# Optimization experiments

Hardware: AMD Instinct MI355X
Metric: run time of the kernel (lower is better)

Reference implementation:

```python
import jax, jax.numpy as jnp
import numpy as np

N, E, ENC, EMB, PI = 100000, 1600000, 128, 128, 98
ALPHA1, ALPHA2 = 0.5, 0.5


def setup_inputs() -> dict:
    key = jax.random.key(0)
    ks = jax.random.split(key, 20)
    s = 0.05
    return {
        "x": jax.random.normal(ks[0], (N, ENC), jnp.float32),
        "d2an": jax.random.normal(ks[1], (N, PI), jnp.float32),
        "ei0": jax.random.randint(ks[2], (2, E), 0, N, jnp.int32),
        "ew0": jax.random.uniform(ks[3], (E,), jnp.float32, 0.1, 4.0),
        "ei1": jax.random.randint(ks[4], (2, E), 0, N, jnp.int32),
        "ew1": jax.random.uniform(ks[5], (E,), jnp.float32, 0.1, 4.0),
        "nodeW1": jax.random.normal(ks[6], (ENC, ENC + PI), jnp.float32) * s,
        "nodeW2": jax.random.normal(ks[7], (ENC, ENC + PI), jnp.float32) * s,
        "W1a": jax.random.normal(ks[8], (EMB, ENC), jnp.float32) * s,
        "W1b": jax.random.normal(ks[9], (EMB, ENC), jnp.float32) * s,
        "W2a": jax.random.normal(ks[10], (EMB, ENC), jnp.float32) * s,
        "W2b": jax.random.normal(ks[11], (EMB, ENC), jnp.float32) * s,
        "W3a": jax.random.normal(ks[12], (EMB, EMB), jnp.float32) * s,
        "W3b": jax.random.normal(ks[13], (EMB, EMB), jnp.float32) * s,
        "W4a": jax.random.normal(ks[14], (EMB, EMB), jnp.float32) * s,
        "W4b": jax.random.normal(ks[15], (EMB, EMB), jnp.float32) * s,
    }


def _layer(x, ei, ew, W1, W2, nodeW, d2an, first):
    """PosKnnGNNLayer.forward: add self loops, optional nodeLin, GCN deg norm +
    edge norm, gather -> lin1/lin2 -> scale -> scatter-add (aggr='add')."""
    n = x.shape[0]
    loop = jnp.arange(n, dtype=ei.dtype)
    row = jnp.concatenate([ei[0], loop])          # source nodes (x_j)
    col = jnp.concatenate([ei[1], loop])          # target nodes (aggregation)
    attr = jnp.concatenate([ew, jnp.ones((n,), ew.dtype)])  # self-loop fill=1.0
    if first:
        x = jnp.concatenate([x, d2an], axis=1) @ nodeW.T
    deg = jax.ops.segment_sum(jnp.ones_like(attr), col, num_segments=n)
    dis = jnp.where(deg > 0, jax.lax.rsqrt(jnp.maximum(deg, 1.0)), 0.0)
    deg_norm = dis[row] * dis[col]                # [E']
    einv = attr ** -0.5
    einv = jnp.where(jnp.isinf(einv), 0.0, einv)
    einv = jnp.minimum(einv, 1.0)                 # clamp >1 to 1
    h1 = x @ W1.T                                 # [N, out]
    h2 = x @ W2.T
    msg = deg_norm[:, None] * h1[row] + einv[:, None] * h2[row]  # [E', out]
    return jax.ops.segment_sum(msg, col, num_segments=n)


def reference(x, d2an, ei0, ew0, ei1, ew1, nodeW1, nodeW2,
              W1a, W1b, W2a, W2b, W3a, W3b, W4a, W4b):
    # eval mode: dropout(p=0.3) is identity
    x0 = jax.nn.relu(_layer(x, ei0, ew0, W1a, W1b, nodeW1, d2an, True))
    x1 = jax.nn.relu(_layer(x, ei1, ew1, W2a, W2b, nodeW2, d2an, True))
    xm = ALPHA1 * x0 + ALPHA2 * x1
    x0 = jax.nn.relu(_layer(xm, ei0, ew0, W3a, W3b, None, None, False))
    x1 = jax.nn.relu(_layer(xm, ei1, ew1, W4a, W4b, None, None, False))
    return ALPHA1 * x0 + ALPHA2 * x1
```

## Files before the change

kernel.cpp:

```cpp
#include <hip/hip_runtime.h>
#include <hip/hip_fp16.h>
#include <stdint.h>

#define NN 100000
#define NE 1600000
#define ETOT (NE + NN)
#define EPB 8192
#define NBLK ((NE + EPB - 1) / EPB)
#define NPB 512
#define NBUK ((NN + NPB - 1) / NPB)

typedef __attribute__((ext_vector_type(8))) short bf16x8;
typedef __attribute__((ext_vector_type(4))) float f32x4;
typedef __attribute__((ext_vector_type(4))) unsigned short us4;

__device__ __forceinline__ float bf2f(unsigned short u) {
    union { unsigned int i; float f; } x; x.i = ((unsigned int)u) << 16; return x.f;
}
__device__ __forceinline__ unsigned short f2bf(float f) {
    union { float f; unsigned int i; } x; x.f = f;
    unsigned int i = x.i;
    return (unsigned short)((i + 0x7FFFu + ((i >> 16) & 1u)) >> 16);
}
__device__ __forceinline__ int packab(float a, float b) {
    unsigned int ua = __half_as_ushort(__float2half_rn(a));
    unsigned int ub = __half_as_ushort(__float2half_rn(b));
    return (int)(ua | (ub << 16));
}
__device__ __forceinline__ float2 unpackab(int p) {
    float a = __half2float(__ushort_as_half((unsigned short)(p & 0xFFFF)));
    float b = __half2float(__ushort_as_half((unsigned short)(((unsigned int)p) >> 16)));
    return make_float2(a, b);
}

__global__ __launch_bounds__(256) void k_cnt(const int* ei0, const int* ei1, int* cntm) {
    __shared__ int h[NBUK];
    const int* col = (blockIdx.y ? ei1 : ei0) + NE;
    for (int i = threadIdx.x; i < NBUK; i += 256) h[i] = 0;
    __syncthreads();
    int base = blockIdx.x * EPB;
    for (int i = 0; i < EPB / 256; i++) {
        int e = base + i * 256 + threadIdx.x;
        if (e < NE) atomicAdd(&h[col[e] >> 9], 1);
    }
    __syncthreads();
    int* out = cntm + ((size_t)blockIdx.y * NBLK + blockIdx.x) * NBUK;
    for (int i = threadIdx.x; i < NBUK; i += 256) out[i] = h[i];
}

__global__ __launch_bounds__(256) void k_btot(const int* cntm, int* bstart, int* btot) {
    __shared__ int s[256];
    int t = threadIdx.x;
    const int* cnt = cntm + (size_t)blockIdx.y * NBLK * NBUK;
    int tot = 0;
    if (t < NBUK)
        for (int blk = 0; blk < NBLK; blk++) tot += cnt[(size_t)blk * NBUK + t];
    s[t] = tot; __syncthreads();
    for (int off = 1; off < 256; off <<= 1) {
        int u = (t >= off) ? s[t - off] : 0;
        __syncthreads(); s[t] += u; __syncthreads();
    }
    if (t < NBUK) {
        bstart[blockIdx.y * NBUK + t] = s[t] - tot;
        btot[blockIdx.y * NBUK + t] = tot;
    }
}

__global__ __launch_bounds__(256) void k_base2(const int* cntm, const int* bstart, int* basem) {
    __shared__ int s[256];
    int b = blockIdx.x;
    const int* cnt = cntm + (size_t)blockIdx.y * NBLK * NBUK;
    int t = threadIdx.x;
    int v = (t < NBLK) ? cnt[(size_t)t * NBUK + b] : 0;
    s[t] = v; __syncthreads();
    for (int off = 1; off < 256; off <<= 1) {
        int u = (t >= off) ? s[t - off] : 0;
        __syncthreads(); s[t] += u; __syncthreads();
    }
    if (t < NBLK)
        basem[((size_t)blockIdx.y * NBLK + t) * NBUK + b] =
            bstart[blockIdx.y * NBUK + b] + (s[t] - v);
}

__global__ __launch_bounds__(256) void k_scat1(const int* ei0, const float* ew0,
                                               const int* ei1, const float* ew1,
                                               const int* basem, int2* st0, int2* st1) {
    __shared__ int lb[NBUK];
    __shared__ int lc[NBUK];
    const int* er = blockIdx.y ? ei1 : ei0;
    const float* ew = blockIdx.y ? ew1 : ew0;
    int2* st = blockIdx.y ? st1 : st0;
    const int* bm = basem + ((size_t)blockIdx.y * NBLK + blockIdx.x) * NBUK;
    for (int i = threadIdx.x; i < NBUK; i += 256) { lb[i] = bm[i]; lc[i] = 0; }
    __syncthreads();
    int base = blockIdx.x * EPB;
    for (int i = 0; i < EPB / 256; i++) {
        int e = base + i * 256 + threadIdx.x;
        if (e >= NE) break;
        int r = er[e];
        int c = er[NE + e];
        float w = ew[e];
        int bkt = c >> 9;
        int rank = atomicAdd(&lc[bkt], 1);
        st[lb[bkt] + rank] = make_int2(r | ((c & 511) << 17), __float_as_int(w));
    }
}

__global__ __launch_bounds__(256) void k_deg(const int* bstart, const int* btot,
                                             const int2* st0, const int2* st1,
                                             int* deg0, int* deg1) {
    __shared__ int h[NPB];
    int b = blockIdx.x;
    const int2* st = blockIdx.y ? st1 : st0;
    int* deg = blockIdx.y ? deg1 : deg0;
    for (int i = threadIdx.x; i < NPB; i += 256) h[i] = 0;
    __syncthreads();
    int s0 = bstart[blockIdx.y * NBUK + b];
    int tot = btot[blockIdx.y * NBUK + b];
    for (int j = s0 + (int)threadIdx.x; j < s0 + tot; j += 256)
        atomicAdd(&h[(st[j].x >> 17) & 511], 1);
    __syncthreads();
    for (int i = threadIdx.x; i < NPB; i += 256) {
        int node = b * NPB + i;
        if (node < NN) deg[node] = h[i] + 1;
    }
}

__global__ void k_scan1(const int* deg0, const int* deg1, int* rp0, int* rp1s, int* bsum) {
    __shared__ int s[256];
    const int* deg = blockIdx.y ? deg1 : deg0;
    int* rp = (blockIdx.y ? rp1s : rp0) + 1;
    int* bs = bsum + blockIdx.y * 128;
    int tid = threadIdx.x;
    int base = blockIdx.x * 1024 + tid * 4;
    int v0 = 0, v1 = 0, v2 = 0, v3 = 0;
    if (base + 0 < NN) v0 = deg[base + 0];
    if (base + 1 < NN) v1 = deg[base + 1];
    if (base + 2 < NN) v2 = deg[base + 2];
    if (base + 3 < NN) v3 = deg[base + 3];
    int sum = v0 + v1 + v2 + v3;
    s[tid] = sum; __syncthreads();
    for (int off = 1; off < 256; off <<= 1) {
        int t = (tid >= off) ? s[tid - off] : 0;
        __syncthreads(); s[tid] += t; __syncthreads();
    }
    int run = s[tid] - sum;
    if (base + 0 < NN) { run += v0; rp[base + 0] = run; }
    if (base + 1 < NN) { run += v1; rp[base + 1] = run; }
    if (base + 2 < NN) { run += v2; rp[base + 2] = run; }
    if (base + 3 < NN) { run += v3; rp[base + 3] = run; }
    if (tid == 255) bs[blockIdx.x] = s[255];
}

__global__ void k_scan2(int* bsum, int nb) {
    __shared__ int s[128];
    int* bs = bsum + blockIdx.x * 128;
    int tid = threadIdx.x;
    int v = (tid < nb) ? bs[tid] : 0;
    s[tid] = v; __syncthreads();
    for (int off = 1; off < 128; off <<= 1) {
        int t = (tid >= off) ? s[tid - off] : 0;
        __syncthreads(); s[tid] += t; __syncthreads();
    }
    if (tid < nb) bs[tid] = s[tid] - v;
}

__global__ void k_scan3(int* rp0, int* rp1s, const int* bsum) {
    int* rowptr = blockIdx.y ? rp1s : rp0;
    int add = bsum[blockIdx.y * 128 + blockIdx.x];
    int tid = threadIdx.x;
    int base = blockIdx.x * 1024 + tid * 4;
    #pragma unroll
    for (int i = 0; i < 4; i++) {
        int idx = base + i;
        if (idx < NN) rowptr[idx + 1] += add;
    }
    if (blockIdx.x == 0 && tid == 0) rowptr[0] = 0;
}

__global__ void k_self(const int* rp0, const int* rp1s, const int* deg0, const int* deg1,
                       int2* eo0, int2* eo1, float* dis0, float* dis1) {
    int i = blockIdx.x * 256 + threadIdx.x;
    if (i >= NN) return;
    const int* rowptr = blockIdx.y ? rp1s : rp0;
    const int* deg = blockIdx.y ? deg1 : deg0;
    int2* eo = blockIdx.y ? eo1 : eo0;
    float* dis = blockIdx.y ? dis1 : dis0;
    int p = rowptr[i];
    float d = (float)deg[i];
    eo[p] = make_int2(i, packab(1.0f / d, 1.0f));
    dis[i] = rsqrtf(d);
}

__global__ __launch_bounds__(256) void k_scat2(const int* rp0, const int* rp1s,
                                               const int* bstart, const int* btot,
                                               const float* dis0, const float* dis1,
                                               const int2* st0, const int2* st1,
                                               int2* eo0, int2* eo1) {
    __shared__ int lcur[NPB];
    __shared__ float ldis[NPB];
    int b = blockIdx.x;
    const int* rowptr = blockIdx.y ? rp1s : rp0;
    const float* dis = blockIdx.y ? dis1 : dis0;
    const int2* st = blockIdx.y ? st1 : st0;
    int2* eo = blockIdx.y ? eo1 : eo0;
    int nstart = b * NPB;
    for (int i = threadIdx.x; i < NPB; i += 256) {
        int node = nstart + i;
        if (node < NN) { lcur[i] = rowptr[node] + 1; ldis[i] = dis[node]; }
    }
    __syncthreads();
    int s0 = bstart[blockIdx.y * NBUK + b];
    int tot = btot[blockIdx.y * NBUK + b];
    for (int j = s0 + (int)threadIdx.x; j < s0 + tot; j += 256) {
        int2 rec = st[j];
        int cl = (rec.x >> 17) & 511;
        int r  = rec.x & 0x1FFFF;
        float w = __int_as_float(rec.y);
        float a = dis[r] * ldis[cl];
        float bb = fminf(rsqrtf(w), 1.0f);
        int pos = atomicAdd(&lcur[cl], 1);
        eo[pos] = make_int2(r, packab(a, bb));
    }
}

__global__ void k_packx(const float* x, const float* d2, unsigned short* Xc) {
    int idx = blockIdx.x * 256 + threadIdx.x;
    if (idx >= NN * 64) return;
    int r = idx >> 6, k4 = (idx & 63) << 2;
    us4 o;
    if (k4 < 128) {
        float4 v = *(const float4*)(x + (size_t)r * 128 + k4);
        o[0] = f2bf(v.x); o[1] = f2bf(v.y); o[2] = f2bf(v.z); o[3] = f2bf(v.w);
    } else {
        #pragma unroll
        for (int i = 0; i < 4; i++) {
            int k = k4 + i;
            float v = (k < 226) ? d2[(size_t)r * 98 + (k - 128)] : 0.f;
            o[i] = f2bf(v);
        }
    }
    *(us4*)(Xc + (size_t)r * 256 + k4) = o;
}

__global__ void k_packw(const float* wn1, const float* wn2,
                        const float* w1a, const float* w1b,
                        const float* w2a, const float* w2b,
                        const float* w3a, const float* w3b,
                        const float* w4a, const float* w4b,
                        unsigned short* Wfnode, unsigned short* WfL) {
    int idx = blockIdx.x * 256 + threadIdx.x;
    if (idx < 65536) {
        int j = idx & 7, lane = (idx >> 3) & 63, ct = (idx >> 9) & 15, ks = idx >> 13;
        int k = ks * 32 + (lane >> 4) * 8 + j;
        int c = ct * 16 + (lane & 15);
        float v = 0.f;
        if (k < 226) v = (c < 128) ? wn1[c * 226 + k] : wn2[(c - 128) * 226 + k];
        Wfnode[idx] = f2bf(v);
    } else if (idx < 196608) {
        int li = idx - 65536;
        int set = li >> 15, r = li & 32767;
        const float* wa = (set == 0) ? w1a : (set == 1) ? w2a : (set == 2) ? w3a : w4a;
        const float* wb = (set == 0) ? w1b : (set == 1) ? w2b : (set == 2) ? w3b : w4b;
        int j = r & 7, lane = (r >> 3) & 63, ct = (r >> 9) & 7, ks = r >> 12;
        int k = ks * 32 + (lane >> 4) * 8 + j;
        int c = ct * 16 + (lane & 15);
        float v = (k < 128) ? wa[c * 128 + k] : wb[c * 128 + (k - 128)];
        WfL[li] = f2bf(v);
    }
}

template <int SRST, int SOFF>
__global__ __launch_bounds__(256) void k_agg(const unsigned short* S,
                                             const int* rowptr, const int2* eg,
                                             unsigned short* G) {
    int c = blockIdx.x * 4 + (threadIdx.x >> 6);
    int lane = threadIdx.x & 63;
    if (c >= NN) return;
    float a0 = 0.f, a1 = 0.f, b0 = 0.f, b1 = 0.f;
    int jb = rowptr[c], je = rowptr[c + 1];
    const unsigned short* Sb = S + SOFF + lane * 2;
    int j = jb;
    for (; j + 16 <= je; j += 16) {
        int2 e[16]; unsigned int u[16];
        #pragma unroll
        for (int i = 0; i < 16; i++) e[i] = eg[j + i];
        #pragma unroll
        for (int i = 0; i < 16; i++)
            u[i] = *(const unsigned int*)(Sb + (size_t)e[i].x * SRST);
        #pragma unroll
        for (int i = 0; i < 16; i++) {
            float2 w = unpackab(e[i].y);
            float x0 = bf2f((unsigned short)(u[i] & 0xFFFF));
            float x1 = bf2f((unsigned short)(u[i] >> 16));
            a0 += w.x * x0; a1 += w.x * x1; b0 += w.y * x0; b1 += w.y * x1;
        }
    }
    for (; j + 4 <= je; j += 4) {
        int2 e[4]; unsigned int u[4];
        #pragma unroll
        for (int i = 0; i < 4; i++) e[i] = eg[j + i];
        #pragma unroll
        for (int i = 0; i < 4; i++)
            u[i] = *(const unsigned int*)(Sb + (size_t)e[i].x * SRST);
        #pragma unroll
        for (int i = 0; i < 4; i++) {
            float2 w = unpackab(e[i].y);
            float x0 = bf2f((unsigned short)(u[i] & 0xFFFF));
            float x1 = bf2f((unsigned short)(u[i] >> 16));
            a0 += w.x * x0; a1 += w.x * x1; b0 += w.y * x0; b1 += w.y * x1;
        }
    }
    for (; j < je; j++) {
        int2 e = eg[j];
        unsigned int u = *(const unsigned int*)(Sb + (size_t)e.x * SRST);
        float2 w = unpackab(e.y);
        float x0 = bf2f((unsigned short)(u & 0xFFFF));
        float x1 = bf2f((unsigned short)(u >> 16));
        a0 += w.x * x0; a1 += w.x * x1; b0 += w.y * x0; b1 += w.y * x1;
    }
    unsigned int* gd = (unsigned int*)(G + (size_t)c * 256);
    gd[lane]      = (unsigned int)f2bf(a0) | ((unsigned int)f2bf(a1) << 16);
    gd[64 + lane] = (unsigned int)f2bf(b0) | ((unsigned int)f2bf(b1) << 16);
}

template <int MODE>
__global__ __launch_bounds__(256) void k_gemm(const unsigned short* A, int arst,
                                              const unsigned short* Wf, int nct_total,
                                              unsigned short* outB, float* outF,
                                              const unsigned short* T, int orst) {
    int wave = threadIdx.x >> 6, lane = threadIdx.x & 63;
    int m = lane & 15, quad = lane >> 4;
    int row0 = blockIdx.x * 64 + wave * 16;
    int arow = row0 + m;
    bool rowok = arow < NN;
    const unsigned short* Ap = A + (size_t)arow * arst + quad * 8;
    int ctbase = blockIdx.y * 8;
    f32x4 acc[8];
    #pragma unroll
    for (int t = 0; t < 8; t++) acc[t] = (f32x4){0.f, 0.f, 0.f, 0.f};

    #pragma unroll
    for (int ks = 0; ks < 8; ks++) {
        bf16x8 a;
        if (rowok) a = *(const bf16x8*)(Ap + ks * 32);
        else       a = (bf16x8){0, 0, 0, 0, 0, 0, 0, 0};
        const unsigned short* wp = Wf + ((size_t)(ks * nct_total + ctbase) * 64 + lane) * 8;
        #pragma unroll
        for (int t = 0; t < 8; t++) {
            bf16x8 b = *(const bf16x8*)(wp + t * 512);
            acc[t] = __builtin_amdgcn_mfma_f32_16x16x32_bf16(a, b, acc[t], 0, 0, 0);
        }
    }

    int col0 = blockIdx.y * 128;
    #pragma unroll
    for (int t = 0; t < 8; t++) {
        int c = col0 + t * 16 + m;
        #pragma unroll
        for (int rg = 0; rg < 4; rg++) {
            int r = row0 + quad * 4 + rg;
            if (r < NN) {
                float v = acc[t][rg];
                if (MODE == 0) {
                    outB[(size_t)r * orst + c] = f2bf(v);
                } else {
                    float tv = bf2f(T[(size_t)r * 128 + c]);
                    float o = 0.5f * fmaxf(tv, 0.f) + 0.5f * fmaxf(v, 0.f);
                    if (MODE == 1) outB[(size_t)r * orst + c] = f2bf(o);
                    else           outF[(size_t)r * 128 + c] = o;
                }
            }
        }
    }
}

extern "C" void kernel_launch(void* const* d_in, const int* in_sizes, int n_in,
                              void* d_out, int out_size, void* d_ws, size_t ws_size,
                              hipStream_t stream) {
    const float* x      = (const float*)d_in[0];
    const float* d2an   = (const float*)d_in[1];
    const int*   ei0    = (const int*)d_in[2];
    const float* ew0    = (const float*)d_in[3];
    const int*   ei1    = (const int*)d_in[4];
    const float* ew1    = (const float*)d_in[5];
    const float* nodeW1 = (const float*)d_in[6];
    const float* nodeW2 = (const float*)d_in[7];
    const float* W1a = (const float*)d_in[8],  *W1b = (const float*)d_in[9];
    const float* W2a = (const float*)d_in[10], *W2b = (const float*)d_in[11];
    const float* W3a = (const float*)d_in[12], *W3b = (const float*)d_in[13];
    const float* W4a = (const float*)d_in[14], *W4b = (const float*)d_in[15];
    float* out = (float*)d_out;

    char* p = (char*)d_ws;
    auto alloc = [&](size_t bytes) -> char* {
        char* r = p; p += (bytes + 255) & ~(size_t)255; return r;
    };
    unsigned short* bufA   = (unsigned short*)alloc((size_t)NN * 256 * 2);
    unsigned short* bufB   = (unsigned short*)alloc((size_t)NN * 256 * 2);
    unsigned short* Tbuf   = (unsigned short*)alloc((size_t)NN * 128 * 2);
    unsigned short* Wfnode = (unsigned short*)alloc(65536 * 2);
    unsigned short* WfL    = (unsigned short*)alloc((size_t)4 * 32768 * 2);
    int*    deg0    = (int*)alloc((size_t)NN * 4);
    int*    deg1    = (int*)alloc((size_t)NN * 4);
    int*    rowptr0 = (int*)alloc((size_t)(NN + 1) * 4);
    int*    rowptr1 = (int*)alloc((size_t)(NN + 1) * 4);
    int*    bsum    = (int*)alloc(2 * 128 * 4);
    float*  dis0    = (float*)alloc((size_t)NN * 4);
    float*  dis1    = (float*)alloc((size_t)NN * 4);
    int2*   eo0     = (int2*)alloc((size_t)ETOT * 8);
    int2*   eo1     = (int2*)alloc((size_t)ETOT * 8);
    int*    cntm    = (int*)alloc((size_t)2 * NBLK * NBUK * 4);
    int*    basem   = (int*)alloc((size_t)2 * NBLK * NBUK * 4);
    int*    btot    = (int*)alloc((size_t)2 * NBUK * 4);
    int*    bstart  = (int*)alloc((size_t)2 * NBUK * 4);

    int2* st0 = (int2*)bufB;
    int2* st1 = st0 + NE;

    int nbN  = (NN + 255) / 256;
    int nbS  = (NN + 1023) / 1024;
    dim3 gP((NN + 63) / 64, 2);
    dim3 gL((NN + 63) / 64, 1);
    int nbA = (NN + 3) / 4;

    k_cnt<<<dim3(NBLK, 2), 256, 0, stream>>>(ei0, ei1, cntm);
    k_btot<<<dim3(1, 2), 256, 0, stream>>>(cntm, bstart, btot);
    k_base2<<<dim3(NBUK, 2), 256, 0, stream>>>(cntm, bstart, basem);
    k_scat1<<<dim3(NBLK, 2), 256, 0, stream>>>(ei0, ew0, ei1, ew1, basem, st0, st1);
    k_deg<<<dim3(NBUK, 2), 256, 0, stream>>>(bstart, btot, st0, st1, deg0, deg1);
    k_scan1<<<dim3(nbS, 2), 256, 0, stream>>>(deg0, deg1, rowptr0, rowptr1, bsum);
    k_scan2<<<2, 128, 0, stream>>>(bsum, nbS);
    k_scan3<<<dim3(nbS, 2), 256, 0, stream>>>(rowptr0, rowptr1, bsum);
    k_self<<<dim3(nbN, 2), 256, 0, stream>>>(rowptr0, rowptr1, deg0, deg1,
                                             eo0, eo1, dis0, dis1);
    k_scat2<<<dim3(NBUK, 2), 256, 0, stream>>>(rowptr0, rowptr1, bstart, btot,
                                               dis0, dis1, st0, st1, eo0, eo1);

    k_packx<<<(NN * 64 + 255) / 256, 256, 0, stream>>>(x, d2an, bufA);
    k_packw<<<768, 256, 0, stream>>>(nodeW1, nodeW2, W1a, W1b, W2a, W2b,
                                     W3a, W3b, W4a, W4b, Wfnode, WfL);

    k_gemm<0><<<gP, 256, 0, stream>>>(bufA, 256, Wfnode, 16, bufB, nullptr, nullptr, 256);
    k_agg<256, 0><<<nbA, 256, 0, stream>>>(bufB, rowptr0, eo0, bufA);
    k_gemm<0><<<gL, 256, 0, stream>>>(bufA, 256, WfL, 8, Tbuf, nullptr, nullptr, 128);
    k_agg<256, 128><<<nbA, 256, 0, stream>>>(bufB, rowptr1, eo1, bufA);
    k_gemm<1><<<gL, 256, 0, stream>>>(bufA, 256, WfL + 32768, 8, bufB, nullptr, Tbuf, 128);

    k_agg<128, 0><<<nbA, 256, 0, stream>>>(bufB, rowptr0, eo0, bufA);
    k_gemm<0><<<gL, 256, 0, stream>>>(bufA, 256, WfL + 2 * 32768, 8, Tbuf, nullptr, nullptr, 128);
    k_agg<128, 0><<<nbA, 256, 0, stream>>>(bufB, rowptr1, eo1, bufA);
    k_gemm<2><<<gL, 256, 0, stream>>>(bufA, 256, WfL + 3 * 32768, 8, nullptr, out, Tbuf, 128);
}
```

Before: 775.4 us.

## Fuse edge aggregation with following GEMM via shared-memory staging

Each aggregation kernel and its following dense GEMM are merged into one kernel. A block of 4 waves aggregates 64 destination rows into swizzled LDS and then runs MFMA on them directly. This removes the global write and read of the aggregated intermediate and halves the kernel launches in the message-passing phase. In exchange, each block now holds 32KB of LDS, only 1563 blocks are launched, and each wave handles 16 rows serially, which lowers latency hiding for the irregular gathers. The buffer roles also change: xm now lives in bufA.

```diff
diff --git a/kernel.cpp b/kernel.cpp
--- a/kernel.cpp
+++ b/kernel.cpp
@@ -270,60 +270,6 @@
     }
 }
 
-template <int SRST, int SOFF>
-__global__ __launch_bounds__(256) void k_agg(const unsigned short* S,
-                                             const int* rowptr, const int2* eg,
-                                             unsigned short* G) {
-    int c = blockIdx.x * 4 + (threadIdx.x >> 6);
-    int lane = threadIdx.x & 63;
-    if (c >= NN) return;
-    float a0 = 0.f, a1 = 0.f, b0 = 0.f, b1 = 0.f;
-    int jb = rowptr[c], je = rowptr[c + 1];
-    const unsigned short* Sb = S + SOFF + lane * 2;
-    int j = jb;
-    for (; j + 16 <= je; j += 16) {
-        int2 e[16]; unsigned int u[16];
-        #pragma unroll
-        for (int i = 0; i < 16; i++) e[i] = eg[j + i];
-        #pragma unroll
-        for (int i = 0; i < 16; i++)
-            u[i] = *(const unsigned int*)(Sb + (size_t)e[i].x * SRST);
-        #pragma unroll
-        for (int i = 0; i < 16; i++) {
-            float2 w = unpackab(e[i].y);
-            float x0 = bf2f((unsigned short)(u[i] & 0xFFFF));
-            float x1 = bf2f((unsigned short)(u[i] >> 16));
-            a0 += w.x * x0; a1 += w.x * x1; b0 += w.y * x0; b1 += w.y * x1;
-        }
-    }
-    for (; j + 4 <= je; j += 4) {
-        int2 e[4]; unsigned int u[4];
-        #pragma unroll
-        for (int i = 0; i < 4; i++) e[i] = eg[j + i];
-        #pragma unroll
-        for (int i = 0; i < 4; i++)
-            u[i] = *(const unsigned int*)(Sb + (size_t)e[i].x * SRST);
-        #pragma unroll
-        for (int i = 0; i < 4; i++) {
-            float2 w = unpackab(e[i].y);
-            float x0 = bf2f((unsigned short)(u[i] & 0xFFFF));
-            float x1 = bf2f((unsigned short)(u[i] >> 16));
-            a0 += w.x * x0; a1 += w.x * x1; b0 += w.y * x0; b1 += w.y * x1;
-        }
-    }
-    for (; j < je; j++) {
-        int2 e = eg[j];
-        unsigned int u = *(const unsigned int*)(Sb + (size_t)e.x * SRST);
-        float2 w = unpackab(e.y);
-        float x0 = bf2f((unsigned short)(u & 0xFFFF));
-        float x1 = bf2f((unsigned short)(u >> 16));
-        a0 += w.x * x0; a1 += w.x * x1; b0 += w.y * x0; b1 += w.y * x1;
-    }
-    unsigned int* gd = (unsigned int*)(G + (size_t)c * 256);
-    gd[lane]      = (unsigned int)f2bf(a0) | ((unsigned int)f2bf(a1) << 16);
-    gd[64 + lane] = (unsigned int)f2bf(b0) | ((unsigned int)f2bf(b1) << 16);
-}
-
 template <int MODE>
 __global__ __launch_bounds__(256) void k_gemm(const unsigned short* A, int arst,
                                               const unsigned short* Wf, int nct_total,
@@ -368,6 +314,106 @@
                     float tv = bf2f(T[(size_t)r * 128 + c]);
                     float o = 0.5f * fmaxf(tv, 0.f) + 0.5f * fmaxf(v, 0.f);
                     if (MODE == 1) outB[(size_t)r * orst + c] = f2bf(o);
+                    else           outF[(size_t)r * 128 + c] = o;
+                }
+            }
+        }
+    }
+}
+
+template <int SRST, int SOFF, int MODE>
+__global__ __launch_bounds__(256) void k_aggemm(const unsigned short* S,
+                                                const int* rowptr, const int2* eg,
+                                                const unsigned short* Wf,
+                                                unsigned short* outB, float* outF,
+                                                const unsigned short* T) {
+    __shared__ unsigned int Gs[64 * 128];
+    int wave = threadIdx.x >> 6, lane = threadIdx.x & 63;
+    int base = blockIdx.x * 64;
+    const unsigned short* Sb = S + SOFF + lane * 2;
+
+    for (int t = 0; t < 16; t++) {
+        int c = base + wave * 16 + t;
+        if (c >= NN) break;
+        float a0 = 0.f, a1 = 0.f, b0 = 0.f, b1 = 0.f;
+        int jb = rowptr[c], je = rowptr[c + 1];
+        int j = jb;
+        for (; j + 16 <= je; j += 16) {
+            int2 e[16]; unsigned int u[16];
+            #pragma unroll
+            for (int i = 0; i < 16; i++) e[i] = eg[j + i];
+            #pragma unroll
+            for (int i = 0; i < 16; i++)
+                u[i] = *(const unsigned int*)(Sb + (size_t)e[i].x * SRST);
+            #pragma unroll
+            for (int i = 0; i < 16; i++) {
+                float2 w = unpackab(e[i].y);
+                float x0 = bf2f((unsigned short)(u[i] & 0xFFFF));
+                float x1 = bf2f((unsigned short)(u[i] >> 16));
+                a0 += w.x * x0; a1 += w.x * x1; b0 += w.y * x0; b1 += w.y * x1;
+            }
+        }
+        for (; j + 4 <= je; j += 4) {
+            int2 e[4]; unsigned int u[4];
+            #pragma unroll
+            for (int i = 0; i < 4; i++) e[i] = eg[j + i];
+            #pragma unroll
+            for (int i = 0; i < 4; i++)
+                u[i] = *(const unsigned int*)(Sb + (size_t)e[i].x * SRST);
+            #pragma unroll
+            for (int i = 0; i < 4; i++) {
+                float2 w = unpackab(e[i].y);
+                float x0 = bf2f((unsigned short)(u[i] & 0xFFFF));
+                float x1 = bf2f((unsigned short)(u[i] >> 16));
+                a0 += w.x * x0; a1 += w.x * x1; b0 += w.y * x0; b1 += w.y * x1;
+            }
+        }
+        for (; j < je; j++) {
+            int2 e = eg[j];
+            unsigned int u = *(const unsigned int*)(Sb + (size_t)e.x * SRST);
+            float2 w = unpackab(e.y);
+            float x0 = bf2f((unsigned short)(u & 0xFFFF));
+            float x1 = bf2f((unsigned short)(u >> 16));
+            a0 += w.x * x0; a1 += w.x * x1; b0 += w.y * x0; b1 += w.y * x1;
+        }
+        int row = wave * 16 + t;
+        int swz = (row & 7) << 2;
+        Gs[(row * 128 + lane) ^ swz]      = (unsigned int)f2bf(a0) | ((unsigned int)f2bf(a1) << 16);
+        Gs[(row * 128 + 64 + lane) ^ swz] = (unsigned int)f2bf(b0) | ((unsigned int)f2bf(b1) << 16);
+    }
+    __syncthreads();
+
+    int m = lane & 15, quad = lane >> 4;
+    int lrow = wave * 16 + m;
+    int swz = (lrow & 7) << 2;
+    f32x4 acc[8];
+    #pragma unroll
+    for (int t = 0; t < 8; t++) acc[t] = (f32x4){0.f, 0.f, 0.f, 0.f};
+    #pragma unroll
+    for (int ks = 0; ks < 8; ks++) {
+        bf16x8 a = *(const bf16x8*)&Gs[(lrow * 128 + quad * 4 + ks * 16) ^ swz];
+        const unsigned short* wp = Wf + ((size_t)(ks * 8) * 64 + lane) * 8;
+        #pragma unroll
+        for (int t = 0; t < 8; t++) {
+            bf16x8 b = *(const bf16x8*)(wp + t * 512);
+            acc[t] = __builtin_amdgcn_mfma_f32_16x16x32_bf16(a, b, acc[t], 0, 0, 0);
+        }
+    }
+    int row0 = base + wave * 16;
+    #pragma unroll
+    for (int t = 0; t < 8; t++) {
+        int c = t * 16 + m;
+        #pragma unroll
+        for (int rg = 0; rg < 4; rg++) {
+            int r = row0 + quad * 4 + rg;
+            if (r < NN) {
+                float v = acc[t][rg];
+                if (MODE == 0) {
+                    outB[(size_t)r * 128 + c] = f2bf(v);
+                } else {
+                    float tv = bf2f(T[(size_t)r * 128 + c]);
+                    float o = 0.5f * fmaxf(tv, 0.f) + 0.5f * fmaxf(v, 0.f);
+                    if (MODE == 1) outB[(size_t)r * 128 + c] = f2bf(o);
                     else           outF[(size_t)r * 128 + c] = o;
                 }
             }
@@ -421,8 +467,7 @@
     int nbN  = (NN + 255) / 256;
     int nbS  = (NN + 1023) / 1024;
     dim3 gP((NN + 63) / 64, 2);
-    dim3 gL((NN + 63) / 64, 1);
-    int nbA = (NN + 3) / 4;
+    int gF = (NN + 63) / 64;
 
     k_cnt<<<dim3(NBLK, 2), 256, 0, stream>>>(ei0, ei1, cntm);
     k_btot<<<dim3(1, 2), 256, 0, stream>>>(cntm, bstart, btot);
@@ -442,13 +487,12 @@
                                      W3a, W3b, W4a, W4b, Wfnode, WfL);
 
     k_gemm<0><<<gP, 256, 0, stream>>>(bufA, 256, Wfnode, 16, bufB, nullptr, nullptr, 256);
-    k_agg<256, 0><<<nbA, 256, 0, stream>>>(bufB, rowptr0, eo0, bufA);
-    k_gemm<0><<<gL, 256, 0, stream>>>(bufA, 256, WfL, 8, Tbuf, nullptr, nullptr, 128);
-    k_agg<256, 128><<<nbA, 256, 0, stream>>>(bufB, rowptr1, eo1, bufA);
-    k_gemm<1><<<gL, 256, 0, stream>>>(bufA, 256, WfL + 32768, 8, bufB, nullptr, Tbuf, 128);
-
-    k_agg<128, 0><<<nbA, 256, 0, stream>>>(bufB, rowptr0, eo0, bufA);
-    k_gemm<0><<<gL, 256, 0, stream>>>(bufA, 256, WfL + 2 * 32768, 8, Tbuf, nullptr, nullptr, 128);
-    k_agg<128, 0><<<nbA, 256, 0, stream>>>(bufB, rowptr1, eo1, bufA);
-    k_gemm<2><<<gL, 256, 0, stream>>>(bufA, 256, WfL + 3 * 32768, 8, nullptr, out, Tbuf, 128);
-}
+    k_aggemm<256, 0, 0><<<gF, 256, 0, stream>>>(bufB, rowptr0, eo0, WfL,
+                                                Tbuf, nullptr, nullptr);
+    k_aggemm<256, 128, 1><<<gF, 256, 0, stream>>>(bufB, rowptr1, eo1, WfL + 32768,
+                                                  bufA, nullptr, Tbuf);
+    k_aggemm<128, 0, 0><<<gF, 256, 0, stream>>>(bufA, rowptr0, eo0, WfL + 2 * 32768,
+                                                Tbuf, nullptr, nullptr);
+    k_aggemm<128, 0, 2><<<gF, 256, 0, stream>>>(bufA, rowptr1, eo1, WfL + 3 * 32768,
+                                                nullptr, out, Tbuf);
+}
```

Measured after the change: 878.8 us. 13.3% more time.
